# Performance work log

Measured on AMD Instinct MI355X. Metric: run time of the kernel, lower is better.

The kernel has to match this reference:

```python
import jax, jax.numpy as jnp
import numpy as np
from jax import lax

# 32 binary morphology kernels, row-major bit strings (kernel01..kernel800)
K3S = ["111001111", "111101101", "111100111", "101101111",
       "011101111", "111101011", "111101110", "110101111"]
K4S = ["0011000110011111", "1100100010011111", "1111100100010011", "1111100110001100",
       "1001100110011111", "1111000100011111", "1111100110011001", "1111100010001111"]
K5S = ["0001100001000011000111111", "1100010000100001000111111",
       "1111110001100001000011000", "1111110001000010000100011",
       "1111110000100001000011111", "1111100001000010000111111",
       "1111110001100011000110001", "1000110001100011000111111"]
K6S = ["000011000001000001000001100001111111", "110000100000100000100000100001111111",
       "111111100001100000100000100000110000", "111111100001000001000001000001000011",
       "111111100000100000100000100000111111", "111111000001000001000001000001111111",
       "111111100001100001100001100001100001", "100001100001100001100001100001111111"]

def _mk(strs, k):
    a = np.array([[int(c) for c in s] for s in strs], dtype=np.float32)
    return jnp.asarray(a.reshape(len(strs), 1, k, k))

# 'thick' mode: enumerate(start=1) vs set(range(32)) drops the LAST kernel (index 31)
GROUPS = [_mk(K3S, 3), _mk(K4S, 4), _mk(K5S, 5), _mk(K6S, 6)[:7]]

DIA = jnp.ones((1, 1, 3, 3), jnp.float32)
ERO = jnp.asarray([[0, 1, 0], [1, 0, 1], [0, 1, 0]], jnp.float32).reshape(1, 1, 3, 3)

def _conv(x, k, pad):
    return lax.conv_general_dilated(x, k, (1, 1), ((pad, pad), (pad, pad)),
                                    dimension_numbers=("NCHW", "OIHW", "NCHW"))

def _sig2(x, beta=0.5, alpha=10.0):
    # 1 / (1 + exp(-alpha*(x - beta)))
    return jax.nn.sigmoid(alpha * (x - beta))

def _endpoints_group(padded, kers):
    # batch all same-size kernels as output channels of one conv
    k = kers.shape[-1]
    pad = k // 2
    nc = _conv(padded, kers, pad)
    nc = nc[:, :, :padded.shape[2], :padded.shape[3]]  # crop (even-size kernels overshoot)
    # soft_threshold(nc, 1.0) * mask
    le = jax.nn.sigmoid(jnp.clip(-10.0 * (nc - 1.0), -10.0, 10.0)) * padded
    return le[:, :, 1:-1, 1:-1].sum(axis=1, keepdims=True)

def _cp_map(t):
    p = jnp.pad(t, ((0, 0), (0, 0), (1, 1), (1, 1)), constant_values=1.0)
    epss = _endpoints_group(p, GROUPS[0])
    for K in GROUPS[1:]:
        epss = epss + _endpoints_group(p, K)
    return _sig2(epss)

def _dilate(x):
    return jnp.clip(_conv(x, DIA, 1), 0.0, 1.0)

def _erode(x):
    t = _conv(x, ERO, 1)
    return _sig2(t / (t.max() + 1e-8), beta=0.7, alpha=10.0)

def _get_cp(t):
    return _dilate(_cp_map(t))

def _topo_loss(pred, gt, num_erosions):
    ge, pe = [gt], [pred]
    for _ in range(num_erosions):
        ge.append(_erode(ge[-1]))
        pe.append(_erode(pe[-1]))
    loss = jnp.float32(0.0)
    for i in range(num_erosions + 1):
        loss = loss + ((_get_cp(pe[i]) - _get_cp(ge[i])) ** 2).sum()
        loss = loss + ((_get_cp(pe[i].max() - pe[i]) - _get_cp(ge[i].max() - ge[i])) ** 2).sum()
    return loss / pred.shape[0]


def setup_inputs() -> dict:
    key = jax.random.key(0)
    k1, k2 = jax.random.split(key)
    B, H, W = 8, 512, 512
    pred = jax.random.uniform(k1, (B, 1, H, W), dtype=jnp.float32)
    gt = jax.random.uniform(k2, (B, 1, H, W), dtype=jnp.float32)
    return {"pred": pred, "gt": gt, "num_erosions": 2}


def reference(pred, gt, num_erosions):
    return _topo_loss(pred, gt, num_erosions)
```

## Files before the change

kernel.cpp:

```cpp
#include <hip/hip_runtime.h>
#include <hip/hip_fp16.h>
#include <cstdint>

static constexpr int B = 8;
static constexpr int H = 512;
static constexpr int W = 512;
static constexpr int HW = H * W;
static constexpr int NPIX = B * HW;
static constexpr int NB1 = 1024;
static constexpr int NBD = 1024;

static constexpr int N_INT = 30 * 14;
static constexpr int N_EDGE = 64 + 120;
static constexpr int GRID_X = N_INT + N_EDGE;

static constexpr float CC = 14.4269504088896f;

__device__ __forceinline__ float rcpf(float x) { return __builtin_amdgcn_rcpf(x); }
__device__ __forceinline__ float exp2f_n(float x) { return __builtin_amdgcn_exp2f(x); }

typedef __attribute__((ext_vector_type(2))) float f2;

__device__ __forceinline__ f2 mk2(float a, float b) { f2 r; r.x = a; r.y = b; return r; }
__device__ __forceinline__ f2 exp2_2(f2 v) {
    f2 r; r.x = exp2f_n(v.x); r.y = exp2f_n(v.y); return r;
}
__device__ __forceinline__ f2 rcp_2(f2 v) {
    f2 r; r.x = rcpf(v.x); r.y = rcpf(v.y); return r;
}
#if defined(__has_builtin)
#if __has_builtin(__builtin_elementwise_fma)
#define FMA2(a, b, c) __builtin_elementwise_fma((a), (b), (c))
#endif
#endif
#ifndef FMA2
__device__ __forceinline__ f2 fma2_(f2 a, f2 b, f2 c) {
    f2 r; r.x = fmaf(a.x, b.x, c.x); r.y = fmaf(a.y, b.y, c.y); return r;
}
#define FMA2(a, b, c) fma2_((a), (b), (c))
#endif

__device__ __forceinline__ float sig_cp(float x) {
    return rcpf(1.0f + exp2f_n(fmaf(x, -CC, 0.5f * CC)));
}
__device__ __forceinline__ float sig_er(float r) {
    return rcpf(1.0f + exp2f_n(fmaf(r, -CC, 0.7f * CC)));
}
__device__ __forceinline__ void pair_term2(f2 nc, f2 negA, f2 s2m,
                                           f2& sd, f2& sc) {
    const f2 CC2 = CC;
    const f2 one2 = 1.0f;
    f2 w = exp2_2(FMA2(nc, CC2, negA));
    sd += rcp_2(FMA2(w, s2m, one2));
    sc += w * rcp_2(w + s2m);
}
__device__ __forceinline__ void end_term2(f2 nc, f2& sd) {
    const f2 CC2 = CC;
    const f2 nCC2 = -CC;
    const f2 one2 = 1.0f;
    sd += rcp_2(one2 + exp2_2(FMA2(nc, CC2, nCC2)));
}
__device__ __forceinline__ float wave_max(float m) {
#pragma unroll
    for (int o = 32; o > 0; o >>= 1) m = fmaxf(m, __shfl_down(m, o, 64));
    return m;
}
__device__ __forceinline__ float wave_sum(float s) {
#pragma unroll
    for (int o = 32; o > 0; o >>= 1) s += __shfl_down(s, o, 64);
    return s;
}

union H4 {
    uint64_t u;
    __half2 h2[2];
    __half h[4];
};

__device__ __forceinline__ float4 h4_to_f4(uint64_t u) {
    H4 v; v.u = u;
    float2 p0 = __half22float2(v.h2[0]);
    float2 p1 = __half22float2(v.h2[1]);
    return make_float4(p0.x, p0.y, p1.x, p1.y);
}
__device__ __forceinline__ float4 f4_add(float4 a, float4 b) {
    return make_float4(a.x + b.x, a.y + b.y, a.z + b.z, a.w + b.w);
}

struct NC2 {
    f2 n3[8], n4[8], n5[8], n6[7];
    f2 v;
};

template <int STRIDE>
__device__ __forceinline__ NC2 sweep2(const f2* rp) {
    NC2 o;
    f2 r2s, r3s, r4s;
    f2 cen0, cen1, cen2, cen3, cen4, cen5, cen6, cen7, cen8;
    {
        f2 c0 = rp[0], c1 = rp[1], c2 = rp[2], c3 = rp[3], c4 = rp[4], c5 = rp[5];
        f2 c45 = c4 + c5, c01 = c0 + c1;
        f2 S6 = (c01 + (c2 + c3)) + c45;
        o.n6[0] = c45; o.n6[1] = c01; o.n6[2] = S6; o.n6[3] = S6;
        o.n6[4] = S6;  o.n6[5] = S6;  o.n6[6] = S6;
    }
    rp += STRIDE;
    {
        f2 c0 = rp[0], c1 = rp[1], c2 = rp[2], c3 = rp[3], c4 = rp[4], c5 = rp[5];
        f2 c45 = c4 + c5, c12 = c1 + c2, c34 = c3 + c4;
        f2 S4 = c12 + c34, S5 = S4 + c5;
        f2 c15 = c1 + c5, c05 = c0 + c5, c14 = c1 + c4;
        o.n6[0] += c5;  o.n6[1] += c0;  o.n6[2] += c05; o.n6[3] += c05;
        o.n6[4] += c0;  o.n6[5] += c5;  o.n6[6] += c05;
        o.n5[0] = c45; o.n5[1] = c12; o.n5[2] = S5; o.n5[3] = S5;
        o.n5[4] = S5;  o.n5[5] = S5;  o.n5[6] = S5; o.n5[7] = c15;
        o.n4[0] = c34; o.n4[1] = c12; o.n4[2] = S4; o.n4[3] = S4;
        o.n4[4] = c14; o.n4[5] = S4;  o.n4[6] = S4; o.n4[7] = S4;
    }
    rp += STRIDE;
    {
        f2 c0 = rp[0], c1 = rp[1], c2 = rp[2], c3 = rp[3], c4 = rp[4], c5 = rp[5];
        f2 c05 = c0 + c5, c15 = c1 + c5, c14 = c1 + c4;
        r2s = (c2 + c3) + c4;
        cen0 = c2; cen1 = c3; cen2 = c4;
        o.n6[0] += c5;  o.n6[1] += c0;  o.n6[2] += c0;  o.n6[3] += c5;
        o.n6[4] += c0;  o.n6[5] += c5;  o.n6[6] += c05;
        o.n5[0] += c5;  o.n5[1] += c1;  o.n5[2] += c15; o.n5[3] += c15;
        o.n5[4] += c1;  o.n5[5] += c5;  o.n5[6] += c15; o.n5[7] += c15;
        o.n4[0] += c4;  o.n4[1] += c1;  o.n4[2] += c14; o.n4[3] += c14;
        o.n4[4] += c14; o.n4[5] += c4;  o.n4[6] += c14; o.n4[7] += c1;
    }
    rp += STRIDE;
    {
        f2 c0 = rp[0], c1 = rp[1], c2 = rp[2], c3 = rp[3], c4 = rp[4], c5 = rp[5];
        f2 c05 = c0 + c5, c15 = c1 + c5, c14 = c1 + c4;
        r3s = (c2 + c3) + c4;
        cen3 = c2; cen4 = c3; cen5 = c4;
        o.v = c3;
        o.n6[0] += c5;  o.n6[1] += c0;  o.n6[2] += c0;  o.n6[3] += c5;
        o.n6[4] += c0;  o.n6[5] += c5;  o.n6[6] += c05;
        o.n5[0] += c5;  o.n5[1] += c1;  o.n5[2] += c1;  o.n5[3] += c5;
        o.n5[4] += c1;  o.n5[5] += c5;  o.n5[6] += c15; o.n5[7] += c15;
        o.n4[0] += c14; o.n4[1] += c14; o.n4[2] += c4;  o.n4[3] += c1;
        o.n4[4] += c14; o.n4[5] += c4;  o.n4[6] += c14; o.n4[7] += c1;
    }
    rp += STRIDE;
    {
        f2 c0 = rp[0], c1 = rp[1], c2 = rp[2], c3 = rp[3], c4 = rp[4], c5 = rp[5];
        f2 c05 = c0 + c5, c15 = c1 + c5, c12 = c1 + c2, c34 = c3 + c4;
        f2 S4 = c12 + c34, c14 = c1 + c4;
        r4s = (c2 + c3) + c4;
        cen6 = c2; cen7 = c3; cen8 = c4;
        o.n6[0] += c05; o.n6[1] += c05; o.n6[2] += c0;  o.n6[3] += c5;
        o.n6[4] += c0;  o.n6[5] += c5;  o.n6[6] += c05;
        o.n5[0] += c15; o.n5[1] += c15; o.n5[2] += c1;  o.n5[3] += c5;
        o.n5[4] += c1;  o.n5[5] += c5;  o.n5[6] += c15; o.n5[7] += c15;
        o.n4[0] += S4;  o.n4[1] += S4;  o.n4[2] += c34; o.n4[3] += c12;
        o.n4[4] += S4;  o.n4[5] += S4;  o.n4[6] += c14; o.n4[7] += S4;
    }
    rp += STRIDE;
    {
        f2 c0 = rp[0], c1 = rp[1], c2 = rp[2], c3 = rp[3], c4 = rp[4], c5 = rp[5];
        f2 c45 = c4 + c5, c12 = c1 + c2;
        f2 t = c3 + c45, S5 = c12 + t, S6 = S5 + c0;
        f2 c01 = c0 + c1, c05 = c0 + c5, c15 = c1 + c5;
        o.n6[0] += S6;  o.n6[1] += S6;  o.n6[2] += c01; o.n6[3] += c45;
        o.n6[4] += S6;  o.n6[5] += S6;  o.n6[6] += c05;
        o.n5[0] += S5;  o.n5[1] += S5;  o.n5[2] += c12; o.n5[3] += c45;
        o.n5[4] += S5;  o.n5[5] += S5;  o.n5[6] += c15; o.n5[7] += S5;
    }
    f2 S33 = (r2s + r3s) + r4s;
    f2 T = S33 - cen4;
    o.n3[0] = T - cen3; o.n3[1] = T - cen7; o.n3[2] = T - cen5; o.n3[3] = T - cen1;
    o.n3[4] = T - cen0; o.n3[5] = T - cen6; o.n3[6] = T - cen8; o.n3[7] = T - cen2;
    return o;
}

__constant__ __device__ const int CI4[8] = {1, 1, 1, 1, 2, 2, 2, 2};
__constant__ __device__ const int CI5[8] = {3, 3, 3, 3, 4, 4, 4, 4};
__constant__ __device__ const int CI6[7] = {4, 4, 4, 4, 5, 5, 5};

template <bool PAIR>
__device__ __forceinline__ void ssum_from_nc2(const NC2& a, const f2* negA,
                                              const f2* s2m, f2& sD, f2& sC) {
    f2 sd = 0.0f, sc = 0.0f;
#pragma unroll
    for (int k = 0; k < 8; k++) {
        if constexpr (PAIR) pair_term2(a.n3[k], negA[0], s2m[0], sd, sc);
        else end_term2(a.n3[k], sd);
    }
#pragma unroll
    for (int k = 0; k < 8; k++) {
        if constexpr (PAIR) pair_term2(a.n4[k], negA[CI4[k]], s2m[CI4[k]], sd, sc);
        else end_term2(a.n4[k], sd);
    }
#pragma unroll
    for (int k = 0; k < 8; k++) {
        if constexpr (PAIR) pair_term2(a.n5[k], negA[CI5[k]], s2m[CI5[k]], sd, sc);
        else end_term2(a.n5[k], sd);
    }
#pragma unroll
    for (int k = 0; k < 7; k++) {
        if constexpr (PAIR) pair_term2(a.n6[k], negA[CI6[k]], s2m[CI6[k]], sd, sc);
        else end_term2(a.n6[k], sd);
    }
    sD = sd;
    sC = sc;
}

__global__ void setup_consts_kernel(const float* __restrict__ S,
                                    float* __restrict__ CST) {
    int t = threadIdx.x;
    if (t < 36) {
        int lvl = t / 12, rem = t % 12, cls = rem >> 1, img = rem & 1;
        const float cntf[6] = {7.0f, 9.0f, 10.0f, 11.0f, 13.0f, 16.0f};
        float M = S[lvl + 3 * img];
        float cm = fmaf(cntf[cls] * M, CC, -CC);
        float m = 0.5f * (cm - CC);
        CST[lvl * 24 + cls * 2 + img] = -(CC + m);
        CST[lvl * 24 + 12 + cls * 2 + img] = exp2f_n(m);
    }
}

__global__ __launch_bounds__(256, 4) void cp_main_kernel(
    const float* __restrict__ x0P, const float* __restrict__ x0G,
    const float* __restrict__ x1P, const float* __restrict__ x1G,
    const float* __restrict__ x2P, const float* __restrict__ x2G,
    const float* __restrict__ S, const float* __restrict__ CST,
    int lvl_base, int plane_lvl0, __half* __restrict__ cp) {
    __shared__ f2 win[37][23];
    const int lvl = lvl_base + (blockIdx.z >> 3);
    const int b = blockIdx.z & 7;
    const float* xP = (lvl == 0) ? x0P : (lvl == 1) ? x1P : x2P;
    const float* xG = (lvl == 0) ? x0G : (lvl == 1) ? x1G : x2G;
    const float MP = S[lvl], MG = S[3 + lvl];
    __half* cpb = cp + (size_t)(4 * (lvl - plane_lvl0)) * NPIX;
    const int tid = threadIdx.y * 16 + threadIdx.x;
    const int ty = threadIdx.y, tx = threadIdx.x;
    const f2* cbase = (const f2*)(CST + lvl * 24);

    if (blockIdx.x < N_INT) {
        const int txB = 1 + (int)blockIdx.x % 30;
        const int tyB = 1 + (int)blockIdx.x / 30;
        const int ox0 = txB * 16, oy0 = tyB * 32;
        const float* pb = xP + b * HW + (oy0 - 3) * W + (ox0 - 3);
        const float* gb = xG + b * HW + (oy0 - 3) * W + (ox0 - 3);
        {
            int i = tid, r = tid / 21, c = tid - (tid / 21) * 21;
            while (i < 37 * 21) {
                win[r][c] = mk2(pb[r * W + c], gb[r * W + c]);
                i += 256; c += 4; r += 12;
                if (c >= 21) { c -= 21; r += 1; }
            }
        }
        __syncthreads();
        f2 negA[6], s2m[6];
#pragma unroll
        for (int c = 0; c < 6; c++) { negA[c] = cbase[c]; s2m[c] = cbase[6 + c]; }
        int o = b * HW + (oy0 + ty) * W + (ox0 + tx);
        {
            f2 sd, sc;
            NC2 a = sweep2<23>(&win[ty][tx]);
            ssum_from_nc2<true>(a, negA, s2m, sd, sc);
            H4 v;
            v.h[0] = __float2half(sig_cp(a.v.x * sd.x));
            v.h[1] = __float2half(sig_cp(a.v.y * sd.y));
            v.h[2] = __float2half(sig_cp((MP - a.v.x) * sc.x));
            v.h[3] = __float2half(sig_cp((MG - a.v.y) * sc.y));
            *(uint64_t*)(cpb + (size_t)o * 4) = v.u;
        }
        o += 16 * W;
        {
            f2 sd, sc;
            NC2 a = sweep2<23>(&win[ty + 16][tx]);
            ssum_from_nc2<true>(a, negA, s2m, sd, sc);
            H4 v;
            v.h[0] = __float2half(sig_cp(a.v.x * sd.x));
            v.h[1] = __float2half(sig_cp(a.v.y * sd.y));
            v.h[2] = __float2half(sig_cp((MP - a.v.x) * sc.x));
            v.h[3] = __float2half(sig_cp((MG - a.v.y) * sc.y));
            *(uint64_t*)(cpb + (size_t)o * 4) = v.u;
        }
    } else {
        const int e = (int)blockIdx.x - N_INT;
        int tx16, ty16;
        if (e < 64) {
            ty16 = e >> 1;
            tx16 = (e & 1) ? 31 : 0;
        } else {
            int e2 = e - 64;
            int r = e2 / 30;
            ty16 = (r == 0) ? 0 : (r == 1) ? 1 : (r == 2) ? 30 : 31;
            tx16 = 1 + e2 % 30;
        }
        const int ox0 = tx16 * 16, oy0 = ty16 * 16;
        const int o = b * HW + (oy0 + ty) * W + (ox0 + tx);
        const bool fastw = (tx16 >= 1) & (tx16 <= 30) & (ty16 >= 1) & (ty16 <= 30);
        if (fastw) {
            const float* pb = xP + b * HW + (oy0 - 3) * W + (ox0 - 3);
            const float* gb = xG + b * HW + (oy0 - 3) * W + (ox0 - 3);
            {
                int i = tid, r = tid / 21, c = tid - (tid / 21) * 21;
                while (i < 21 * 21) {
                    win[r][c] = mk2(pb[r * W + c], gb[r * W + c]);
                    i += 256; c += 4; r += 12;
                    if (c >= 21) { c -= 21; r += 1; }
                }
            }
            __syncthreads();
            f2 negA[6], s2m[6], sd, sc;
#pragma unroll
            for (int c = 0; c < 6; c++) { negA[c] = cbase[c]; s2m[c] = cbase[6 + c]; }
            NC2 a = sweep2<23>(&win[ty][tx]);
            ssum_from_nc2<true>(a, negA, s2m, sd, sc);
            H4 v;
            v.h[0] = __float2half(sig_cp(a.v.x * sd.x));
            v.h[1] = __float2half(sig_cp(a.v.y * sd.y));
            v.h[2] = __float2half(sig_cp((MP - a.v.x) * sc.x));
            v.h[3] = __float2half(sig_cp((MG - a.v.y) * sc.y));
            *(uint64_t*)(cpb + (size_t)o * 4) = v.u;
        } else {
            const float* pb = xP + b * HW;
            const float* gb = xG + b * HW;
            {
                int i = tid, r = tid / 21, c = tid - (tid / 21) * 21;
                while (i < 21 * 21) {
                    int pr = oy0 - 2 + r;
                    int pc = ox0 - 2 + c;
                    f2 v;
                    if (pr < 0 || pr > H + 1 || pc < 0 || pc > W + 1) {
                        v = 0.0f;
                    } else if (pr == 0 || pr == H + 1 || pc == 0 || pc == W + 1) {
                        v = 1.0f;
                    } else {
                        v = mk2(pb[(pr - 1) * W + (pc - 1)], gb[(pr - 1) * W + (pc - 1)]);
                    }
                    win[r][c] = v;
                    i += 256; c += 4; r += 12;
                    if (c >= 21) { c -= 21; r += 1; }
                }
            }
            __syncthreads();
            f2 sd, sc, junk;
            NC2 a = sweep2<23>(&win[ty][tx]);
            ssum_from_nc2<false>(a, nullptr, nullptr, sd, junk);
            f2 vD = a.v;
            __half2* po = (__half2*)(cpb + (size_t)o * 4);
            po[0] = __halves2half2(__float2half(sig_cp(vD.x * sd.x)),
                                   __float2half(sig_cp(vD.y * sd.y)));
            __syncthreads();
            {
                int i = tid, r = tid / 21, c = tid - (tid / 21) * 21;
                while (i < 21 * 21) {
                    int pr = oy0 - 2 + r;
                    int pc = ox0 - 2 + c;
                    f2 v;
                    if (pr < 0 || pr > H + 1 || pc < 0 || pc > W + 1) {
                        v = 0.0f;
                    } else if (pr == 0 || pr == H + 1 || pc == 0 || pc == W + 1) {
                        v = 1.0f;
                    } else {
                        v = mk2(MP - pb[(pr - 1) * W + (pc - 1)],
                                MG - gb[(pr - 1) * W + (pc - 1)]);
                    }
                    win[r][c] = v;
                    i += 256; c += 4; r += 12;
                    if (c >= 21) { c -= 21; r += 1; }
                }
            }
            __syncthreads();
            NC2 ac = sweep2<23>(&win[ty][tx]);
            ssum_from_nc2<false>(ac, nullptr, nullptr, sc, junk);
            po[1] = __halves2half2(__float2half(sig_cp(ac.v.x * sc.x)),
                                   __float2half(sig_cp(ac.v.y * sc.y)));
        }
    }
}

__global__ __launch_bounds__(256, 4) void dil_diff2_kernel(
    const __half* __restrict__ cp, float* __restrict__ partial) {
    const int plane_grp = blockIdx.x >> 9;
    const int r = blockIdx.x & 511;
    const __half* cpb = cp + (size_t)(4 * plane_grp) * NPIX;
    const int x0 = threadIdx.x << 1;
    const int y0 = (r & 63) << 3;
    const int b = r >> 6;
    const __half* pb = cpb + (size_t)b * HW * 4;

    float4 ring0[3], ring1[3];
    float s = 0.0f;
#pragma unroll
    for (int j = 0; j < 10; j++) {
        int yy = y0 - 1 + j;
        float4 a0 = make_float4(0.f, 0.f, 0.f, 0.f);
        float4 a1 = a0;
        if (yy >= 0 && yy < H) {
            const __half* row = pb + (size_t)yy * (W * 4);
            float4 f0 = h4_to_f4(*(const uint64_t*)(row + (size_t)x0 * 4));
            float4 f1 = h4_to_f4(*(const uint64_t*)(row + (size_t)(x0 + 1) * 4));
            float4 lf = make_float4(0.f, 0.f, 0.f, 0.f), rt = lf;
            if (x0 > 0)
                lf = h4_to_f4(*(const uint64_t*)(row + (size_t)(x0 - 1) * 4));
            if (x0 + 2 < W)
                rt = h4_to_f4(*(const uint64_t*)(row + (size_t)(x0 + 2) * 4));
            a0 = f4_add(f4_add(lf, f0), f1);
            a1 = f4_add(f4_add(f0, f1), rt);
        }
        ring0[j % 3] = a0; ring1[j % 3] = a1;
        if (j >= 2) {
            float4 v0 = f4_add(f4_add(ring0[(j - 2) % 3], ring0[(j - 1) % 3]),
                               ring0[j % 3]);
            float4 v1 = f4_add(f4_add(ring1[(j - 2) % 3], ring1[(j - 1) % 3]),
                               ring1[j % 3]);
            float d1 = fminf(v0.x, 1.0f) - fminf(v0.y, 1.0f);
            float d2 = fminf(v0.z, 1.0f) - fminf(v0.w, 1.0f);
            s += fmaf(d1, d1, d2 * d2);
            d1 = fminf(v1.x, 1.0f) - fminf(v1.y, 1.0f);
            d2 = fminf(v1.z, 1.0f) - fminf(v1.w, 1.0f);
            s += fmaf(d1, d1, d2 * d2);
        }
    }
    s = wave_sum(s);
    __shared__ float red[4];
    int tid = threadIdx.x;
    if ((tid & 63) == 0) red[tid >> 6] = s;
    __syncthreads();
    if (tid == 0) partial[blockIdx.x] = (red[0] + red[1]) + (red[2] + red[3]);
}

__device__ __forceinline__ void cross4(const float* __restrict__ xp, int idx,
                                       int y, int c, float4& ctr, float t[4]) {
    const float4* v = (const float4*)(xp + idx);
    ctr = v[0];
    float4 up = (y > 0) ? *(const float4*)(xp + idx - W)
                        : make_float4(0, 0, 0, 0);
    float4 dn = (y < H - 1) ? *(const float4*)(xp + idx + W)
                            : make_float4(0, 0, 0, 0);
    float lf = (c > 0) ? xp[idx - 1] : 0.0f;
    float rt = (c < W - 4) ? xp[idx + 4] : 0.0f;
    t[0] = (up.x + dn.x) + (lf + ctr.y);
    t[1] = (up.y + dn.y) + (ctr.x + ctr.z);
    t[2] = (up.z + dn.z) + (ctr.y + ctr.w);
    t[3] = (up.w + dn.w) + (ctr.z + rt);
}

__global__ __launch_bounds__(256) void cross_max_both_kernel(
    const float* __restrict__ xP, const float* __restrict__ xG,
    float4* __restrict__ partial) {
    float mtP = 0, mtG = 0, mrP = 0, mrG = 0;
    for (int T = blockIdx.x * 256 + threadIdx.x; T < NPIX / 4; T += NB1 * 256) {
        int idx = T * 4;
        int i = idx & (HW - 1);
        int y = i >> 9;
        int c = i & (W - 1);
        float4 ctr;
        float t[4];
        cross4(xP, idx, y, c, ctr, t);
        mtP = fmaxf(mtP, fmaxf(fmaxf(t[0], t[1]), fmaxf(t[2], t[3])));
        mrP = fmaxf(mrP, fmaxf(fmaxf(ctr.x, ctr.y), fmaxf(ctr.z, ctr.w)));
        cross4(xG, idx, y, c, ctr, t);
        mtG = fmaxf(mtG, fmaxf(fmaxf(t[0], t[1]), fmaxf(t[2], t[3])));
        mrG = fmaxf(mrG, fmaxf(fmaxf(ctr.x, ctr.y), fmaxf(ctr.z, ctr.w)));
    }
    mtP = wave_max(mtP); mtG = wave_max(mtG);
    mrP = wave_max(mrP); mrG = wave_max(mrG);
    __shared__ float red[4][4];
    int tid = threadIdx.x;
    if ((tid & 63) == 0) {
        int w = tid >> 6;
        red[w][0] = mtP; red[w][1] = mtG; red[w][2] = mrP; red[w][3] = mrG;
    }
    __syncthreads();
    if (tid == 0) {
        float4 r;
        r.x = fmaxf(fmaxf(red[0][0], red[1][0]), fmaxf(red[2][0], red[3][0]));
        r.y = fmaxf(fmaxf(red[0][1], red[1][1]), fmaxf(red[2][1], red[3][1]));
        r.z = fmaxf(fmaxf(red[0][2], red[1][2]), fmaxf(red[2][2], red[3][2]));
        r.w = fmaxf(fmaxf(red[0][3], red[1][3]), fmaxf(red[2][3], red[3][3]));
        partial[blockIdx.x] = r;
    }
}

__global__ __launch_bounds__(256) void erode_both_kernel(
    const float* __restrict__ xP, const float* __restrict__ xG,
    const float4* __restrict__ PM,
    float* __restrict__ yP, float* __restrict__ yG,
    float* ymaxP, float* ymaxG, float* rmaxP, float* rmaxG) {
    float a = 0, bm = 0, c4 = 0, d4 = 0;
    {
        int t = threadIdx.x;
#pragma unroll
        for (int k = 0; k < NB1 / 256; k++) {
            float4 p = PM[t + k * 256];
            a = fmaxf(a, p.x); bm = fmaxf(bm, p.y);
            c4 = fmaxf(c4, p.z); d4 = fmaxf(d4, p.w);
        }
        a = wave_max(a); bm = wave_max(bm); c4 = wave_max(c4); d4 = wave_max(d4);
        __shared__ float red[4][4];
        if ((t & 63) == 0) {
            int w = t >> 6;
            red[w][0] = a; red[w][1] = bm; red[w][2] = c4; red[w][3] = d4;
        }
        __syncthreads();
        a  = fmaxf(fmaxf(red[0][0], red[1][0]), fmaxf(red[2][0], red[3][0]));
        bm = fmaxf(fmaxf(red[0][1], red[1][1]), fmaxf(red[2][1], red[3][1]));
        c4 = fmaxf(fmaxf(red[0][2], red[1][2]), fmaxf(red[2][2], red[3][2]));
        d4 = fmaxf(fmaxf(red[0][3], red[1][3]), fmaxf(red[2][3], red[3][3]));
    }
    const float tP_max = a, tG_max = bm;
    const float invP = rcpf(tP_max + 1e-8f);
    const float invG = rcpf(tG_max + 1e-8f);

    const int T = blockIdx.x * 256 + threadIdx.x;
    if (T < NPIX / 4) {
        int idx = T * 4;
        int i = idx & (HW - 1);
        int y = i >> 9;
        int c = i & (W - 1);
        float4 ctr;
        float t[4], o[4];
        cross4(xP, idx, y, c, ctr, t);
#pragma unroll
        for (int k = 0; k < 4; k++) o[k] = sig_er(t[k] * invP);
        *(float4*)(yP + idx) = make_float4(o[0], o[1], o[2], o[3]);
        cross4(xG, idx, y, c, ctr, t);
#pragma unroll
        for (int k = 0; k < 4; k++) o[k] = sig_er(t[k] * invG);
        *(float4*)(yG + idx) = make_float4(o[0], o[1], o[2], o[3]);
    }
    if (blockIdx.x == 0 && threadIdx.x == 0) {
        *ymaxP = sig_er(tP_max * invP);
        *ymaxG = sig_er(tG_max * invG);
        *rmaxP = c4;
        *rmaxG = d4;
    }
}

__global__ __launch_bounds__(1024) void finalize_kernel(
    const float* __restrict__ PS, float* out) {
    int t = threadIdx.x;
    float s = PS[t] + ((t < 512) ? PS[t + 1024] : 0.0f);
    s = wave_sum(s);
    __shared__ float red[16];
    if ((t & 63) == 0) red[t >> 6] = s;
    __syncthreads();
    if (t == 0) {
        float tot = 0.0f;
#pragma unroll
        for (int i = 0; i < 16; i++) tot += red[i];
        out[0] = tot * (1.0f / (float)B);
    }
}

extern "C" void kernel_launch(void* const* d_in, const int* in_sizes, int n_in,
                              void* d_out, int out_size, void* d_ws, size_t ws_size,
                              hipStream_t stream) {
    (void)in_sizes; (void)n_in; (void)out_size;
    const float* pred = (const float*)d_in[0];
    const float* gt   = (const float*)d_in[1];
    float* out = (float*)d_out;

    float* S  = (float*)d_ws;
    float4* PM = (float4*)(S + 64);
    float* CST = S + 64;
    float* PS = S + 64 + 4 * NB1;
    float* P1 = PS + 3 * NBD;
    float* G1 = P1 + NPIX;
    float* P2 = G1 + NPIX;
    float* G2 = P2 + NPIX;
    __half* CP = (__half*)(G2 + NPIX);

    const size_t base_b = (size_t)(64 + 4 * NB1 + 3 * NBD) * 4 +
                          (size_t)4 * NPIX * 4;
    const bool merged = ws_size >= base_b + (size_t)12 * NPIX * 2;

    const dim3 b1(256), g1(NB1), gE(NPIX / 4 / 256);
    const dim3 b2(16, 16, 1);

    cross_max_both_kernel<<<g1, b1, 0, stream>>>(pred, gt, PM);
    erode_both_kernel<<<gE, b1, 0, stream>>>(pred, gt, PM, P1, G1,
                                             S + 1, S + 4, S + 0, S + 3);
    cross_max_both_kernel<<<g1, b1, 0, stream>>>(P1, G1, PM);
    erode_both_kernel<<<gE, b1, 0, stream>>>(P1, G1, PM, P2, G2,
                                             S + 2, S + 5, S + 12, S + 13);
    setup_consts_kernel<<<1, 64, 0, stream>>>(S, CST);

    if (merged) {
        cp_main_kernel<<<dim3(GRID_X, 1, 3 * B), b2, 0, stream>>>(
            pred, gt, P1, G1, P2, G2, S, CST, 0, 0, CP);
        dil_diff2_kernel<<<dim3(3 * 512), b1, 0, stream>>>(CP, PS);
    } else {
        for (int lvl = 0; lvl < 3; lvl++) {
            cp_main_kernel<<<dim3(GRID_X, 1, B), b2, 0, stream>>>(
                pred, gt, P1, G1, P2, G2, S, CST, lvl, lvl, CP);
            dil_diff2_kernel<<<dim3(512), b1, 0, stream>>>(CP, PS + lvl * 512);
        }
    }

    finalize_kernel<<<1, 1024, 0, stream>>>(PS, out);
}
```

Baseline: 256.2 us.

## Fuse first erosion with second cross-max pass and fold constant setup into erode

A new erode_cmax kernel computes the first erosion for a 4-row band, halo rows included, into LDS. It then reduces the cross-sum and raw maxima of that eroded band directly from LDS, so the separate cross_max pass that re-read P1/G1 from global memory is gone. The setup_consts kernel is folded into block 0 of the second erode kernel, which removes one more launch. The cost is recomputing the halo rows of the erosion and placing the PM2 partials inside the CP buffer, which is only written afterwards.

```diff
diff --git a/kernel.cpp b/kernel.cpp
--- a/kernel.cpp
+++ b/kernel.cpp
@@ -206,20 +206,6 @@
     }
     sD = sd;
     sC = sc;
-}
-
-__global__ void setup_consts_kernel(const float* __restrict__ S,
-                                    float* __restrict__ CST) {
-    int t = threadIdx.x;
-    if (t < 36) {
-        int lvl = t / 12, rem = t % 12, cls = rem >> 1, img = rem & 1;
-        const float cntf[6] = {7.0f, 9.0f, 10.0f, 11.0f, 13.0f, 16.0f};
-        float M = S[lvl + 3 * img];
-        float cm = fmaf(cntf[cls] * M, CC, -CC);
-        float m = 0.5f * (cm - CC);
-        CST[lvl * 24 + cls * 2 + img] = -(CC + m);
-        CST[lvl * 24 + 12 + cls * 2 + img] = exp2f_n(m);
-    }
 }
 
 __global__ __launch_bounds__(256, 4) void cp_main_kernel(
@@ -444,6 +430,20 @@
     t[3] = (up.w + dn.w) + (ctr.z + rt);
 }
 
+__device__ __forceinline__ void cross_lds(const float* rm1, const float* r0,
+                                          const float* rp1, int col,
+                                          float4& ctr, float t[4]) {
+    ctr = *(const float4*)(r0 + col);
+    float4 up = *(const float4*)(rm1 + col);
+    float4 dn = *(const float4*)(rp1 + col);
+    float lf = (col > 0) ? r0[col - 1] : 0.0f;
+    float rt = (col < W - 4) ? r0[col + 4] : 0.0f;
+    t[0] = (up.x + dn.x) + (lf + ctr.y);
+    t[1] = (up.y + dn.y) + (ctr.x + ctr.z);
+    t[2] = (up.z + dn.z) + (ctr.y + ctr.w);
+    t[3] = (up.w + dn.w) + (ctr.z + rt);
+}
+
 __global__ __launch_bounds__(256) void cross_max_both_kernel(
     const float* __restrict__ xP, const float* __restrict__ xG,
     float4* __restrict__ partial) {
@@ -481,11 +481,103 @@
     }
 }
 
+__global__ __launch_bounds__(256) void erode_cmax_kernel(
+    const float* __restrict__ xP, const float* __restrict__ xG,
+    const float4* __restrict__ PM1,
+    float* __restrict__ yP, float* __restrict__ yG,
+    float4* __restrict__ PMo, float* __restrict__ S) {
+    __shared__ float lyP[6][W], lyG[6][W];
+    __shared__ float red[4][4];
+    const int tid = threadIdx.x;
+    const int b = blockIdx.x >> 7;
+    const int y0 = ((int)blockIdx.x & 127) << 2;
+
+    float a = 0, bm = 0, c4 = 0, d4 = 0;
+#pragma unroll
+    for (int k = 0; k < NB1 / 256; k++) {
+        float4 p = PM1[tid + k * 256];
+        a = fmaxf(a, p.x); bm = fmaxf(bm, p.y);
+        c4 = fmaxf(c4, p.z); d4 = fmaxf(d4, p.w);
+    }
+    a = wave_max(a); bm = wave_max(bm); c4 = wave_max(c4); d4 = wave_max(d4);
+    if ((tid & 63) == 0) {
+        int w = tid >> 6;
+        red[w][0] = a; red[w][1] = bm; red[w][2] = c4; red[w][3] = d4;
+    }
+    __syncthreads();
+    a  = fmaxf(fmaxf(red[0][0], red[1][0]), fmaxf(red[2][0], red[3][0]));
+    bm = fmaxf(fmaxf(red[0][1], red[1][1]), fmaxf(red[2][1], red[3][1]));
+    c4 = fmaxf(fmaxf(red[0][2], red[1][2]), fmaxf(red[2][2], red[3][2]));
+    d4 = fmaxf(fmaxf(red[0][3], red[1][3]), fmaxf(red[2][3], red[3][3]));
+    const float invP = rcpf(a + 1e-8f);
+    const float invG = rcpf(bm + 1e-8f);
+
+    for (int t = tid; t < 6 * 128; t += 256) {
+        int ri = t >> 7;
+        int col = (t & 127) << 2;
+        int yy = y0 - 1 + ri;
+        float4 oP = make_float4(0.f, 0.f, 0.f, 0.f), oG = oP;
+        if (yy >= 0 && yy < H) {
+            int idx = b * HW + yy * W + col;
+            float4 ctr; float tv[4];
+            cross4(xP, idx, yy, col, ctr, tv);
+            oP = make_float4(sig_er(tv[0] * invP), sig_er(tv[1] * invP),
+                             sig_er(tv[2] * invP), sig_er(tv[3] * invP));
+            cross4(xG, idx, yy, col, ctr, tv);
+            oG = make_float4(sig_er(tv[0] * invG), sig_er(tv[1] * invG),
+                             sig_er(tv[2] * invG), sig_er(tv[3] * invG));
+            if (ri >= 1 && ri <= 4) {
+                *(float4*)(yP + idx) = oP;
+                *(float4*)(yG + idx) = oG;
+            }
+        }
+        *(float4*)(&lyP[ri][col]) = oP;
+        *(float4*)(&lyG[ri][col]) = oG;
+    }
+    __syncthreads();
+
+    float mtP = 0, mtG = 0, mrP = 0, mrG = 0;
+    for (int t = tid; t < 4 * 128; t += 256) {
+        int rj = 1 + (t >> 7);
+        int col = (t & 127) << 2;
+        float4 ctr; float tv[4];
+        cross_lds(lyP[rj - 1], lyP[rj], lyP[rj + 1], col, ctr, tv);
+        mtP = fmaxf(mtP, fmaxf(fmaxf(tv[0], tv[1]), fmaxf(tv[2], tv[3])));
+        mrP = fmaxf(mrP, fmaxf(fmaxf(ctr.x, ctr.y), fmaxf(ctr.z, ctr.w)));
+        cross_lds(lyG[rj - 1], lyG[rj], lyG[rj + 1], col, ctr, tv);
+        mtG = fmaxf(mtG, fmaxf(fmaxf(tv[0], tv[1]), fmaxf(tv[2], tv[3])));
+        mrG = fmaxf(mrG, fmaxf(fmaxf(ctr.x, ctr.y), fmaxf(ctr.z, ctr.w)));
+    }
+    mtP = wave_max(mtP); mtG = wave_max(mtG);
+    mrP = wave_max(mrP); mrG = wave_max(mrG);
+    __syncthreads();
+    if ((tid & 63) == 0) {
+        int w = tid >> 6;
+        red[w][0] = mtP; red[w][1] = mtG; red[w][2] = mrP; red[w][3] = mrG;
+    }
+    __syncthreads();
+    if (tid == 0) {
+        float4 r;
+        r.x = fmaxf(fmaxf(red[0][0], red[1][0]), fmaxf(red[2][0], red[3][0]));
+        r.y = fmaxf(fmaxf(red[0][1], red[1][1]), fmaxf(red[2][1], red[3][1]));
+        r.z = fmaxf(fmaxf(red[0][2], red[1][2]), fmaxf(red[2][2], red[3][2]));
+        r.w = fmaxf(fmaxf(red[0][3], red[1][3]), fmaxf(red[2][3], red[3][3]));
+        PMo[blockIdx.x] = r;
+        if (blockIdx.x == 0) {
+            S[1] = sig_er(a * invP);
+            S[4] = sig_er(bm * invG);
+            S[0] = c4;
+            S[3] = d4;
+        }
+    }
+}
+
 __global__ __launch_bounds__(256) void erode_both_kernel(
     const float* __restrict__ xP, const float* __restrict__ xG,
     const float4* __restrict__ PM,
     float* __restrict__ yP, float* __restrict__ yG,
-    float* ymaxP, float* ymaxG, float* rmaxP, float* rmaxG) {
+    float* ymaxP, float* ymaxG, float* rmaxP, float* rmaxG,
+    const float* __restrict__ Sg, float* __restrict__ CST) {
     float a = 0, bm = 0, c4 = 0, d4 = 0;
     {
         int t = threadIdx.x;
@@ -528,11 +620,27 @@
         for (int k = 0; k < 4; k++) o[k] = sig_er(t[k] * invG);
         *(float4*)(yG + idx) = make_float4(o[0], o[1], o[2], o[3]);
     }
-    if (blockIdx.x == 0 && threadIdx.x == 0) {
-        *ymaxP = sig_er(tP_max * invP);
-        *ymaxG = sig_er(tG_max * invG);
-        *rmaxP = c4;
-        *rmaxG = d4;
+    if (blockIdx.x == 0) {
+        if (threadIdx.x == 0) {
+            *ymaxP = sig_er(tP_max * invP);
+            *ymaxG = sig_er(tG_max * invG);
+            *rmaxP = c4;
+            *rmaxG = d4;
+        }
+        if (threadIdx.x < 36) {
+            int t = threadIdx.x;
+            int lvl = t / 12, rem = t % 12, cls = rem >> 1, img = rem & 1;
+            const float cntf[6] = {7.0f, 9.0f, 10.0f, 11.0f, 13.0f, 16.0f};
+            float M;
+            if (lvl == 2)
+                M = img ? sig_er(tG_max * invG) : sig_er(tP_max * invP);
+            else
+                M = Sg[lvl + 3 * img];
+            float cm = fmaf(cntf[cls] * M, CC, -CC);
+            float m = 0.5f * (cm - CC);
+            CST[lvl * 24 + cls * 2 + img] = -(CC + m);
+            CST[lvl * 24 + 12 + cls * 2 + img] = exp2f_n(m);
+        }
     }
 }
 
@@ -562,13 +670,14 @@
 
     float* S  = (float*)d_ws;
     float4* PM = (float4*)(S + 64);
-    float* CST = S + 64;
     float* PS = S + 64 + 4 * NB1;
+    float* CST = PS + 2560;
     float* P1 = PS + 3 * NBD;
     float* G1 = P1 + NPIX;
     float* P2 = G1 + NPIX;
     float* G2 = P2 + NPIX;
     __half* CP = (__half*)(G2 + NPIX);
+    float4* PM2 = (float4*)CP;
 
     const size_t base_b = (size_t)(64 + 4 * NB1 + 3 * NBD) * 4 +
                           (size_t)4 * NPIX * 4;
@@ -578,12 +687,11 @@
     const dim3 b2(16, 16, 1);
 
     cross_max_both_kernel<<<g1, b1, 0, stream>>>(pred, gt, PM);
-    erode_both_kernel<<<gE, b1, 0, stream>>>(pred, gt, PM, P1, G1,
-                                             S + 1, S + 4, S + 0, S + 3);
-    cross_max_both_kernel<<<g1, b1, 0, stream>>>(P1, G1, PM);
-    erode_both_kernel<<<gE, b1, 0, stream>>>(P1, G1, PM, P2, G2,
-                                             S + 2, S + 5, S + 12, S + 13);
-    setup_consts_kernel<<<1, 64, 0, stream>>>(S, CST);
+    erode_cmax_kernel<<<dim3(NB1), b1, 0, stream>>>(pred, gt, PM, P1, G1,
+                                                    PM2, S);
+    erode_both_kernel<<<gE, b1, 0, stream>>>(P1, G1, PM2, P2, G2,
+                                             S + 2, S + 5, S + 12, S + 13,
+                                             S, CST);
 
     if (merged) {
         cp_main_kernel<<<dim3(GRID_X, 1, 3 * B), b2, 0, stream>>>(
```

Measured after the change: 251.6 us. About the same (-1.8%).
